# Kernel tuning notes

Hardware: AMD Instinct MI355X
Metric: run time of the kernel (lower is better)

## Reference

```python
import jax, jax.numpy as jnp
import numpy as np

N_HEAD = 16
R = 4  # reciprocal rank

def setup_inputs() -> dict:
    key = jax.random.key(0)
    ks = jax.random.split(key, 8)
    B, T, C = 2, 2048, 1024
    H = N_HEAD
    D = C // H
    D_std = D - R
    x = jax.random.normal(ks[0], (B, T, C), dtype=jnp.float32)
    W_attn = jax.random.normal(ks[1], (3 * C, C), dtype=jnp.float32) * (1.0 / np.sqrt(C))
    W_proj = jax.random.normal(ks[2], (C, C), dtype=jnp.float32) * (1.0 / np.sqrt(C))
    w_std = jnp.full((H,), D_std / D, dtype=jnp.float32)
    w_rec = jnp.full((H,), R / D, dtype=jnp.float32)
    skip_std = jnp.float32(2.0)
    skip_low = jnp.float32(-3.0)
    rwr_alpha = jnp.full((H,), 0.05, dtype=jnp.float32)
    return {"x": x, "W_attn": W_attn, "W_proj": W_proj, "w_std": w_std,
            "w_rec": w_rec, "skip_std": skip_std, "skip_low": skip_low,
            "rwr_alpha": rwr_alpha}

def reference(x, W_attn, W_proj, w_std, w_rec, skip_std, skip_low, rwr_alpha):
    B, T, C = x.shape
    H = N_HEAD
    D = C // H
    D_std = D - R
    # fused QKV projection: [Qf | Kf | V]
    fused = jnp.einsum('btc,fc->btf', x, W_attn)
    qf, kf, v = jnp.split(fused, 3, axis=-1)
    Qf = qf.reshape(B, T, H, D).transpose(0, 2, 1, 3)  # (B,H,T,D)
    Kf = kf.reshape(B, T, H, D).transpose(0, 2, 1, 3)
    V = v.reshape(B, T, H, D).transpose(0, 2, 1, 3)
    # dynamic per-head gate scaling folded into Qf/Kf
    g_std = jnp.sqrt(jnp.clip(w_std * jax.nn.sigmoid(skip_std), 1e-8))  # (H,)
    g_rec = jnp.sqrt(jnp.clip(w_rec * jax.nn.sigmoid(skip_low), 1e-8))  # (H,)
    scale = jnp.concatenate([
        jnp.broadcast_to(g_std[:, None], (H, D_std)),
        jnp.broadcast_to(g_rec[:, None], (H, R)),
    ], axis=-1)  # (H, D)
    scale = scale[None, :, None, :]  # (1,H,1,D)
    Qf = Qf * scale
    Kf = Kf * scale
    # causal SDPA (scale = 1/sqrt(head_dim), dropout=0)
    scores = jnp.einsum('bhqd,bhkd->bhqk', Qf, Kf) / jnp.sqrt(jnp.float32(D))
    causal = jnp.tril(jnp.ones((T, T), dtype=bool))
    scores = jnp.where(causal[None, None], scores, jnp.float32(-1e30))
    attn = jax.nn.softmax(scores, axis=-1)
    y = jnp.einsum('bhqk,bhkd->bhqd', attn, V)
    # self-restart mix: out = (1-alpha)*attn_out + alpha*V, alpha in [0, 0.5]
    alpha = jnp.clip(rwr_alpha, 0.0, 0.5)[None, :, None, None]
    y = (1.0 - alpha) * y + alpha * V
    y = y.transpose(0, 2, 1, 3).reshape(B, T, C)
    return jnp.einsum('btc,oc->bto', y, W_proj)
```

## Files before the change

### kernel.cpp

```cpp
#include <hip/hip_runtime.h>
#include <hip/hip_bf16.h>
#include <math.h>
#include <stdint.h>

#define B_    2
#define T_    2048
#define C_    1024
#define H_    16
#define D_    64
#define R_    4
#define DSTD  60
#define F_    3072
#define BT_   (B_ * T_)

#define LOG2E 1.44269504088896340736f

typedef __bf16 bf16x8 __attribute__((ext_vector_type(8)));
typedef __bf16 bf16x4 __attribute__((ext_vector_type(4)));
typedef float  f32x4  __attribute__((ext_vector_type(4)));

__device__ __forceinline__ int swz(int row, int blk) {
    return blk ^ ((row >> 1) & 7);
}

__device__ __forceinline__ void st_pair(__bf16* p, __bf16 a, __bf16 b) {
    union { __bf16 h[2]; uint32_t u; } t;
    t.h[0] = a; t.h[1] = b;
    *(uint32_t*)p = t.u;
}

__device__ __forceinline__ void gload_lds16(const void* g, void* l) {
    __builtin_amdgcn_global_load_lds(
        (const __attribute__((address_space(1))) uint32_t*)g,
        (__attribute__((address_space(3))) uint32_t*)l, 16, 0, 0);
}

__global__ __launch_bounds__(256) void cast3_kernel(
    const float* __restrict__ a, int na4,
    const float* __restrict__ b, int nb4,
    const float* __restrict__ c, int nc4,
    __bf16* __restrict__ oa, __bf16* __restrict__ ob, __bf16* __restrict__ oc)
{
    int i = blockIdx.x * 256 + threadIdx.x;
    const float* s; __bf16* d; int j = i;
    if (j < na4) { s = a; d = oa; }
    else {
        j -= na4;
        if (j < nb4) { s = b; d = ob; }
        else {
            j -= nb4;
            if (j >= nc4) return;
            s = c; d = oc;
        }
    }
    float4 v = ((const float4*)s)[j];
    bf16x4 o;
    o[0] = (__bf16)v.x; o[1] = (__bf16)v.y;
    o[2] = (__bf16)v.z; o[3] = (__bf16)v.w;
    ((bf16x4*)d)[j] = o;
}

__global__ __launch_bounds__(256) void gemm_qkv_kernel(
    const __bf16* __restrict__ A,
    const __bf16* __restrict__ Bw,
    const float* __restrict__ w_std, const float* __restrict__ w_rec,
    const float* __restrict__ skip_std, const float* __restrict__ skip_low,
    __bf16* __restrict__ Q, __bf16* __restrict__ K, __bf16* __restrict__ V)
{
    __shared__ __bf16 As[128 * 32];
    __shared__ __bf16 Bs[128 * 32];

    const int tid  = threadIdx.x;
    const int row0 = blockIdx.x * 128;
    const int col0 = blockIdx.y * 128;

    const int w    = tid >> 6;
    const int lane = tid & 63;
    const int quad = lane >> 4;
    const int lt   = lane & 15;
    const int wm   = w >> 1;
    const int wn   = w & 1;

    const int lrow = tid >> 2;
    const int lcol = (tid & 3) * 8;

    f32x4 acc[4][4];
#pragma unroll
    for (int i = 0; i < 4; ++i)
#pragma unroll
        for (int j = 0; j < 4; ++j)
#pragma unroll
            for (int r = 0; r < 4; ++r) acc[i][j][r] = 0.f;

    for (int kt = 0; kt < C_ / 32; ++kt) {
        const int k0 = kt * 32;
        __syncthreads();
#pragma unroll
        for (int rr = 0; rr < 2; ++rr) {
            gload_lds16(A  + (size_t)(row0 + rr * 64 + lrow) * C_ + k0 + lcol,
                        As + rr * 2048 + tid * 8);
            gload_lds16(Bw + (size_t)(col0 + rr * 64 + lrow) * C_ + k0 + lcol,
                        Bs + rr * 2048 + tid * 8);
        }
        __syncthreads();

        bf16x8 af[4], bf[4];
#pragma unroll
        for (int i = 0; i < 4; ++i)
            af[i] = *(const bf16x8*)&As[(wm * 64 + i * 16 + lt) * 32 + quad * 8];
#pragma unroll
        for (int j = 0; j < 4; ++j)
            bf[j] = *(const bf16x8*)&Bs[(wn * 64 + j * 16 + lt) * 32 + quad * 8];
#pragma unroll
        for (int i = 0; i < 4; ++i)
#pragma unroll
            for (int j = 0; j < 4; ++j)
                acc[i][j] = __builtin_amdgcn_mfma_f32_16x16x32_bf16(af[i], bf[j], acc[i][j], 0, 0, 0);
    }

    const int colbase = col0 + wn * 64;
    const int which   = colbase >> 10;
    const int h       = (colbase & (C_ - 1)) >> 6;

    const float ss = 1.f / (1.f + __expf(-skip_std[0]));
    const float sl = 1.f / (1.f + __expf(-skip_low[0]));
    const float gs = sqrtf(fmaxf(w_std[h] * ss, 1e-8f));
    const float gr = sqrtf(fmaxf(w_rec[h] * sl, 1e-8f));

    __bf16* dstM = (which == 0) ? Q : (which == 1) ? K : V;

#pragma unroll
    for (int i = 0; i < 4; ++i) {
#pragma unroll
        for (int r = 0; r < 4; ++r) {
            const int row = row0 + wm * 64 + i * 16 + quad * 4 + r;
            const int b = row >> 11;
            const int t = row & (T_ - 1);
            __bf16* dp = dstM + (((size_t)b * H_ + h) * T_ + t) * D_;
#pragma unroll
            for (int j = 0; j < 4; ++j) {
                const int d = j * 16 + lt;
                float val = acc[i][j][r];
                if (which == 0)      val *= ((d < DSTD) ? gs : gr) * (0.125f * LOG2E);
                else if (which == 1) val *= (d < DSTD) ? gs : gr;
                dp[d] = (__bf16)val;
            }
        }
    }
}

__global__ __launch_bounds__(256) void gemm_out_kernel(
    const __bf16* __restrict__ A,
    const __bf16* __restrict__ Bw,
    float* __restrict__ out)
{
    __shared__ __bf16 As[128 * 32];
    __shared__ __bf16 Bs[128 * 32];

    const int tid  = threadIdx.x;
    const int row0 = blockIdx.x * 128;
    const int col0 = blockIdx.y * 128;

    const int w    = tid >> 6;
    const int lane = tid & 63;
    const int quad = lane >> 4;
    const int lt   = lane & 15;
    const int wm   = w >> 1;
    const int wn   = w & 1;

    const int lrow = tid >> 2;
    const int lcol = (tid & 3) * 8;

    f32x4 acc[4][4];
#pragma unroll
    for (int i = 0; i < 4; ++i)
#pragma unroll
        for (int j = 0; j < 4; ++j)
#pragma unroll
            for (int r = 0; r < 4; ++r) acc[i][j][r] = 0.f;

    for (int kt = 0; kt < C_ / 32; ++kt) {
        const int k0 = kt * 32;
        __syncthreads();
#pragma unroll
        for (int rr = 0; rr < 2; ++rr) {
            gload_lds16(A  + (size_t)(row0 + rr * 64 + lrow) * C_ + k0 + lcol,
                        As + rr * 2048 + tid * 8);
            gload_lds16(Bw + (size_t)(col0 + rr * 64 + lrow) * C_ + k0 + lcol,
                        Bs + rr * 2048 + tid * 8);
        }
        __syncthreads();

        bf16x8 af[4], bf[4];
#pragma unroll
        for (int i = 0; i < 4; ++i)
            af[i] = *(const bf16x8*)&As[(wm * 64 + i * 16 + lt) * 32 + quad * 8];
#pragma unroll
        for (int j = 0; j < 4; ++j)
            bf[j] = *(const bf16x8*)&Bs[(wn * 64 + j * 16 + lt) * 32 + quad * 8];
#pragma unroll
        for (int i = 0; i < 4; ++i)
#pragma unroll
            for (int j = 0; j < 4; ++j)
                acc[i][j] = __builtin_amdgcn_mfma_f32_16x16x32_bf16(af[i], bf[j], acc[i][j], 0, 0, 0);
    }

#pragma unroll
    for (int i = 0; i < 4; ++i)
#pragma unroll
        for (int r = 0; r < 4; ++r) {
            const int row = row0 + wm * 64 + i * 16 + quad * 4 + r;
            float* op = out + (size_t)row * C_ + col0 + wn * 64 + lt;
#pragma unroll
            for (int j = 0; j < 4; ++j)
                op[j * 16] = acc[i][j][r];
        }
}

__global__ __launch_bounds__(256) void attn_kernel(
    const __bf16* __restrict__ Q, const __bf16* __restrict__ K,
    const __bf16* __restrict__ V, const float* __restrict__ rwr_alpha,
    __bf16* __restrict__ Y)
{
    __shared__ __align__(16) __bf16 Ks[2][64][64];
    __shared__ __align__(16) __bf16 Vt[2][64][64];
    __shared__ __align__(16) __bf16 Ps[4][16][64];

    const int tid = threadIdx.x;
    const int bh  = blockIdx.x & 31;
    const int g   = blockIdx.x >> 5;
    const int qt  = (g < 8) ? (31 - g) : (g < 16) ? (g - 8)
                  : (g < 24) ? (39 - g) : (g - 16);
    const int h   = bh & (H_ - 1);
    const int b   = bh >> 4;

    const __bf16* Qb = Q + (((size_t)b * H_ + h) * T_) * D_;
    const __bf16* Kb = K + (((size_t)b * H_ + h) * T_) * D_;
    const __bf16* Vb = V + (((size_t)b * H_ + h) * T_) * D_;

    const int w    = tid >> 6;
    const int lane = tid & 63;
    const int quad = lane >> 4;
    const int lt   = lane & 15;

    const int kp = (tid >> 3) * 2;
    const int dc = (tid & 7) * 8;
    const int kblk = kp >> 3, koff = kp & 7;

    const __bf16* qrow = Qb + (size_t)(qt * 64 + w * 16 + lt) * D_;
    bf16x8 qf[2];
    qf[0] = *(const bf16x8*)(qrow + quad * 8);
    qf[1] = *(const bf16x8*)(qrow + 32 + quad * 8);

    bf16x8 ones;
#pragma unroll
    for (int u = 0; u < 8; ++u) ones[u] = (__bf16)1.0f;

    {
        const __bf16* ks = Kb + (size_t)kp * 64 + dc;
        const __bf16* vs = Vb + (size_t)kp * 64 + dc;
        bf16x8 k1 = *(const bf16x8*)(ks);
        bf16x8 k2 = *(const bf16x8*)(ks + 64);
        bf16x8 v1 = *(const bf16x8*)(vs);
        bf16x8 v2 = *(const bf16x8*)(vs + 64);
        *(bf16x8*)&Ks[0][kp    ][swz(kp, dc >> 3) * 8] = k1;
        *(bf16x8*)&Ks[0][kp + 1][swz(kp, dc >> 3) * 8] = k2;
#pragma unroll
        for (int u = 0; u < 8; ++u) {
            const int row = dc + u;
            st_pair(&Vt[0][row][swz(row, kblk) * 8 + koff], v1[u], v2[u]);
        }
    }
    __syncthreads();

    f32x4 lacc;
    f32x4 oacc[4];
#pragma unroll
    for (int r = 0; r < 4; ++r) lacc[r] = 0.f;
#pragma unroll
    for (int n = 0; n < 4; ++n)
#pragma unroll
        for (int r = 0; r < 4; ++r) oacc[n][r] = 0.f;

    for (int kt = 0; kt <= qt; ++kt) {
        const int cur = kt & 1;
        const bool pre = (kt < qt);

        bf16x8 k1, k2, v1, v2;
        if (pre) {
            const __bf16* ks = Kb + (size_t)(kt + 1) * 4096 + (size_t)kp * 64 + dc;
            const __bf16* vs = Vb + (size_t)(kt + 1) * 4096 + (size_t)kp * 64 + dc;
            k1 = *(const bf16x8*)(ks);
            k2 = *(const bf16x8*)(ks + 64);
            v1 = *(const bf16x8*)(vs);
            v2 = *(const bf16x8*)(vs + 64);
        }

        f32x4 sacc[4];
#pragma unroll
        for (int n = 0; n < 4; ++n)
#pragma unroll
            for (int r = 0; r < 4; ++r) sacc[n][r] = 0.f;
#pragma unroll
        for (int kk = 0; kk < 2; ++kk) {
#pragma unroll
            for (int n = 0; n < 4; ++n) {
                const int row = n * 16 + lt;
                bf16x8 bk = *(const bf16x8*)&Ks[cur][row][swz(row, kk * 4 + quad) * 8];
                sacc[n] = __builtin_amdgcn_mfma_f32_16x16x32_bf16(qf[kk], bk, sacc[n], 0, 0, 0);
            }
        }

        if (kt == qt) {
            const int lq = w * 16 + quad * 4;
#pragma unroll
            for (int n = 0; n < 4; ++n) {
                const int col = n * 16 + lt;
#pragma unroll
                for (int r = 0; r < 4; ++r)
                    if (col > lq + r) sacc[n][r] = -1e30f;
            }
        }

#pragma unroll
        for (int r = 0; r < 4; ++r) {
            const int prow = quad * 4 + r;
#pragma unroll
            for (int n = 0; n < 4; ++n) {
                const float p = exp2f(sacc[n][r]);
                Ps[w][prow][swz(prow, n * 2 + (lt >> 3)) * 8 + (lt & 7)] = (__bf16)p;
            }
        }

#pragma unroll
        for (int kk = 0; kk < 2; ++kk) {
            bf16x8 ap = *(const bf16x8*)&Ps[w][lt][swz(lt, kk * 4 + quad) * 8];
            lacc = __builtin_amdgcn_mfma_f32_16x16x32_bf16(ap, ones, lacc, 0, 0, 0);
#pragma unroll
            for (int nd = 0; nd < 4; ++nd) {
                const int drow = nd * 16 + lt;
                bf16x8 bv = *(const bf16x8*)&Vt[cur][drow][swz(drow, kk * 4 + quad) * 8];
                oacc[nd] = __builtin_amdgcn_mfma_f32_16x16x32_bf16(ap, bv, oacc[nd], 0, 0, 0);
            }
        }

        {
            const float lm = fmaxf(fmaxf(lacc[0], lacc[1]), fmaxf(lacc[2], lacc[3]));
            if (__ballot(lm > 1.0e12f)) {
                const float sc = 1.0f / 4294967296.0f;
#pragma unroll
                for (int r = 0; r < 4; ++r) lacc[r] *= sc;
#pragma unroll
                for (int n = 0; n < 4; ++n)
#pragma unroll
                    for (int r = 0; r < 4; ++r) oacc[n][r] *= sc;
            }
        }

        if (pre) {
            const int nxt = 1 - cur;
            *(bf16x8*)&Ks[nxt][kp    ][swz(kp, dc >> 3) * 8] = k1;
            *(bf16x8*)&Ks[nxt][kp + 1][swz(kp, dc >> 3) * 8] = k2;
#pragma unroll
            for (int u = 0; u < 8; ++u) {
                const int row = dc + u;
                st_pair(&Vt[nxt][row][swz(row, kblk) * 8 + koff], v1[u], v2[u]);
            }
        }
        __syncthreads();
    }

    const float a = fminf(fmaxf(rwr_alpha[h], 0.f), 0.5f);
#pragma unroll
    for (int r = 0; r < 4; ++r) {
        const float inv = 1.f / lacc[r];
        const int qg = qt * 64 + w * 16 + quad * 4 + r;
        const __bf16* vp = Vb + (size_t)qg * D_;
        __bf16* yp = Y + ((size_t)(b * T_ + qg)) * C_ + h * D_;
#pragma unroll
        for (int nd = 0; nd < 4; ++nd) {
            const int d = nd * 16 + lt;
            yp[d] = (__bf16)((1.f - a) * oacc[nd][r] * inv + a * (float)vp[d]);
        }
    }
}

extern "C" void kernel_launch(void* const* d_in, const int* in_sizes, int n_in,
                              void* d_out, int out_size, void* d_ws, size_t ws_size,
                              hipStream_t stream) {
    const float* x        = (const float*)d_in[0];
    const float* W_attn   = (const float*)d_in[1];
    const float* W_proj   = (const float*)d_in[2];
    const float* w_std    = (const float*)d_in[3];
    const float* w_rec    = (const float*)d_in[4];
    const float* skip_std = (const float*)d_in[5];
    const float* skip_low = (const float*)d_in[6];
    const float* rwr      = (const float*)d_in[7];
    float* out = (float*)d_out;

    const size_t nX  = (size_t)BT_ * C_;
    const size_t nWa = (size_t)F_ * C_;
    const size_t nWp = (size_t)C_ * C_;
    const size_t per = (size_t)B_ * H_ * T_ * D_;

    __bf16* xb  = (__bf16*)d_ws;
    __bf16* Wab = xb  + nX;
    __bf16* Wpb = Wab + nWa;
    __bf16* Qb  = Wpb + nWp;
    __bf16* Kb  = Qb  + per;
    __bf16* Vb  = Kb  + per;
    __bf16* Yb  = Vb  + per;

    const int na4 = nX / 4, nb4 = nWa / 4, nc4 = nWp / 4;
    cast3_kernel<<<dim3((na4 + nb4 + nc4 + 255) / 256), 256, 0, stream>>>(
        x, na4, W_attn, nb4, W_proj, nc4, xb, Wab, Wpb);

    gemm_qkv_kernel<<<dim3(BT_ / 128, F_ / 128), 256, 0, stream>>>(
        xb, Wab, w_std, w_rec, skip_std, skip_low, Qb, Kb, Vb);
    attn_kernel<<<dim3(32 * (T_ / 64)), 256, 0, stream>>>(Qb, Kb, Vb, rwr, Yb);
    gemm_out_kernel<<<dim3(BT_ / 128, C_ / 128), 256, 0, stream>>>(Yb, Wpb, out);
}
```

Measured before the change: 191.6 us.

## Load K tiles directly to LDS and transpose S MFMA for vectorized P stores

K tiles for the attention loop are now copied from global memory straight into swizzled LDS with direct-to-LDS loads, so they no longer pass through registers and separate LDS stores. The QK^T MFMA operands are swapped so each lane holds four consecutive keys for one query, which lets the P tile be written to LDS as a single 4-wide bf16 store per n instead of scalar stores. The causal mask indexing is updated to match. This relies on gload_lds16 (defined elsewhere) being issued correctly with the barrier, and on that barrier ordering the async LDS writes before the buffer is read.

```diff
diff --git a/kernel.cpp b/kernel.cpp
--- a/kernel.cpp
+++ b/kernel.cpp
@@ -243,6 +243,11 @@
     const int quad = lane >> 4;
     const int lt   = lane & 15;
 
+    const int kr0 = tid >> 3;
+    const int kc0 = (tid & 7) ^ ((kr0 >> 1) & 7);
+    const int kr1 = 32 + kr0;
+    const int kc1 = (tid & 7) ^ ((kr1 >> 1) & 7);
+
     const int kp = (tid >> 3) * 2;
     const int dc = (tid & 7) * 8;
     const int kblk = kp >> 3, koff = kp & 7;
@@ -256,15 +261,12 @@
 #pragma unroll
     for (int u = 0; u < 8; ++u) ones[u] = (__bf16)1.0f;
 
+    gload_lds16(Kb + (size_t)kr0 * 64 + kc0 * 8, &Ks[0][0][0] + tid * 8);
+    gload_lds16(Kb + (size_t)kr1 * 64 + kc1 * 8, &Ks[0][32][0] + tid * 8);
     {
-        const __bf16* ks = Kb + (size_t)kp * 64 + dc;
         const __bf16* vs = Vb + (size_t)kp * 64 + dc;
-        bf16x8 k1 = *(const bf16x8*)(ks);
-        bf16x8 k2 = *(const bf16x8*)(ks + 64);
         bf16x8 v1 = *(const bf16x8*)(vs);
         bf16x8 v2 = *(const bf16x8*)(vs + 64);
-        *(bf16x8*)&Ks[0][kp    ][swz(kp, dc >> 3) * 8] = k1;
-        *(bf16x8*)&Ks[0][kp + 1][swz(kp, dc >> 3) * 8] = k2;
 #pragma unroll
         for (int u = 0; u < 8; ++u) {
             const int row = dc + u;
@@ -284,14 +286,15 @@
 
     for (int kt = 0; kt <= qt; ++kt) {
         const int cur = kt & 1;
+        const int nxt = 1 - cur;
         const bool pre = (kt < qt);
 
-        bf16x8 k1, k2, v1, v2;
+        bf16x8 v1, v2;
         if (pre) {
-            const __bf16* ks = Kb + (size_t)(kt + 1) * 4096 + (size_t)kp * 64 + dc;
-            const __bf16* vs = Vb + (size_t)(kt + 1) * 4096 + (size_t)kp * 64 + dc;
-            k1 = *(const bf16x8*)(ks);
-            k2 = *(const bf16x8*)(ks + 64);
+            const size_t toff = (size_t)(kt + 1) * 4096;
+            gload_lds16(Kb + toff + (size_t)kr0 * 64 + kc0 * 8, &Ks[nxt][0][0] + tid * 8);
+            gload_lds16(Kb + toff + (size_t)kr1 * 64 + kc1 * 8, &Ks[nxt][32][0] + tid * 8);
+            const __bf16* vs = Vb + toff + (size_t)kp * 64 + dc;
             v1 = *(const bf16x8*)(vs);
             v2 = *(const bf16x8*)(vs + 64);
         }
@@ -306,30 +309,28 @@
 #pragma unroll
             for (int n = 0; n < 4; ++n) {
                 const int row = n * 16 + lt;
-                bf16x8 bk = *(const bf16x8*)&Ks[cur][row][swz(row, kk * 4 + quad) * 8];
-                sacc[n] = __builtin_amdgcn_mfma_f32_16x16x32_bf16(qf[kk], bk, sacc[n], 0, 0, 0);
+                bf16x8 ak = *(const bf16x8*)&Ks[cur][row][swz(row, kk * 4 + quad) * 8];
+                sacc[n] = __builtin_amdgcn_mfma_f32_16x16x32_bf16(ak, qf[kk], sacc[n], 0, 0, 0);
             }
         }
 
         if (kt == qt) {
-            const int lq = w * 16 + quad * 4;
+            const int ql = w * 16 + lt;
 #pragma unroll
             for (int n = 0; n < 4; ++n) {
-                const int col = n * 16 + lt;
+                const int keyb = n * 16 + quad * 4;
 #pragma unroll
                 for (int r = 0; r < 4; ++r)
-                    if (col > lq + r) sacc[n][r] = -1e30f;
-            }
-        }
-
-#pragma unroll
-        for (int r = 0; r < 4; ++r) {
-            const int prow = quad * 4 + r;
-#pragma unroll
-            for (int n = 0; n < 4; ++n) {
-                const float p = exp2f(sacc[n][r]);
-                Ps[w][prow][swz(prow, n * 2 + (lt >> 3)) * 8 + (lt & 7)] = (__bf16)p;
-            }
+                    if (keyb + r > ql) sacc[n][r] = -1e30f;
+            }
+        }
+
+#pragma unroll
+        for (int n = 0; n < 4; ++n) {
+            bf16x4 pv;
+#pragma unroll
+            for (int r = 0; r < 4; ++r) pv[r] = (__bf16)exp2f(sacc[n][r]);
+            *(bf16x4*)&Ps[w][lt][swz(lt, n * 2 + (quad >> 1)) * 8 + (quad & 1) * 4] = pv;
         }
 
 #pragma unroll
@@ -358,9 +359,6 @@
         }
 
         if (pre) {
-            const int nxt = 1 - cur;
-            *(bf16x8*)&Ks[nxt][kp    ][swz(kp, dc >> 3) * 8] = k1;
-            *(bf16x8*)&Ks[nxt][kp + 1][swz(kp, dc >> 3) * 8] = k2;
 #pragma unroll
             for (int u = 0; u < 8; ++u) {
                 const int row = dc + u;
```

Result: faster. 187.2 us (-2.3%).
